# Kernel optimization log

Hardware: AMD Instinct MI355X
Metric: run time of the kernel (lower is better)

The kernel has to match this reference:

```python
import jax, jax.numpy as jnp
import numpy as np

ALPHA1 = 0.1   # rank margin
ALPHA2 = 5.0   # penalty scale when violated
ALPHA3 = 10.0  # sigmoid sharpness
ALPHA_OTHER = 0.5  # floor for top-k threshold


def setup_inputs() -> dict:
    key = jax.random.key(0)
    B, C, L, S = 4096, 9605, 8, 50  # batch, classes, whitelist labels, classes per label
    k1, k2, k3 = jax.random.split(key, 3)
    x = jax.random.normal(k1, (B, C), dtype=jnp.float32)
    # sparse multi-label binarized targets (~10 positives/sample)
    y = (jax.random.uniform(k2, (B, C)) < 0.001).astype(jnp.float32)
    y_neg = (jax.random.uniform(k3, (B, C)) < 0.001).astype(jnp.float32)
    # disjoint per-label whitelist class index sets -> [L, C] boolean masks
    rng = np.random.default_rng(0)
    idx = rng.choice(C, size=L * S, replace=False).reshape(L, S)
    wl = np.zeros((L, C), dtype=bool)
    wl[np.arange(L)[:, None], idx] = True
    return {"x": x, "y": y, "y_neg": y_neg, "wl_mask": jnp.asarray(wl)}


def reference(x, y, y_neg, wl_mask):
    # x, y, y_neg: [B, C]; wl_mask: [L, C] bool. Returns scalar loss_rank_all.sum().
    # (The per-element BCE `loss` tensor and find_gt_whitelist(y_neg) in the
    #  original are dead code w.r.t. the returned value and are omitted.)
    xs = jax.nn.sigmoid(x)                                   # [B, C]
    wl_f = wl_mask.astype(x.dtype)                           # [L, C]
    # gt label present iff sum of y over that label's whitelist indices > 0
    gt_mask = (y @ wl_f.T) > 0                               # [B, L]
    has_gt = jnp.any(gt_mask, axis=1)                        # [B]
    first_gt = jnp.argmax(gt_mask, axis=1)                   # [B] first gt label
    # x_sorted[15] (16th largest) via top_k instead of full sort
    top16 = jax.lax.top_k(xs, 16)[0][:, 15]                  # [B]
    thres = jnp.maximum(top16, ALPHA_OTHER)                  # [B]
    # ---- branch: no gt whitelist label ----
    union = jnp.any(wl_mask, axis=0)                         # [C]
    x2_no = jnp.max(jnp.where(union[None, :], xs, -jnp.inf), axis=1)
    x1_no = thres
    # ---- branch: has gt whitelist label ----
    samp_mask = wl_mask[first_gt]                            # [B, C]
    x1_gt = jnp.max(jnp.where(samp_mask, xs, -jnp.inf), axis=1)
    L = wl_mask.shape[0]
    # faithful to original: indexes xs at LABEL positions 0..L-1, init 0
    non_gt = jnp.max(jnp.where(~gt_mask, xs[:, :L], 0.0), axis=1, initial=0.0)
    x2_gt = jnp.maximum(non_gt, thres)
    # ---- select branch and apply our_rank_loss ----
    x1 = jnp.where(has_gt, x1_gt, x1_no)
    x2 = jnp.where(has_gt, x2_gt, x2_no)
    d = x2 - x1 + ALPHA1
    sig = jax.nn.sigmoid(ALPHA3 * d)
    rank = jnp.where(d > 0, ALPHA2 * sig, sig)
    return jnp.sum(rank)
```

## Files before the change

### kernel.cpp

```cpp
#include <hip/hip_runtime.h>
#include <stdint.h>

#define BLOCK 512
#define CAP 512
#define LISTCAP 2048
#define WS_ROUT 2560
static constexpr int LBL = 8;

#define A1 0.1f
#define A2 5.0f
#define A3 10.0f

__device__ __forceinline__ unsigned b2key(unsigned u) {
  return (u & 0x80000000u) ? ~u : (u | 0x80000000u);
}
__device__ __forceinline__ unsigned f2key(float f) { return b2key(__float_as_uint(f)); }
__device__ __forceinline__ float key2f(unsigned k) {
  unsigned u = (k & 0x80000000u) ? (k & 0x7FFFFFFFu) : ~k;
  return __uint_as_float(u);
}
__device__ __forceinline__ float sigm(float v) { return 1.0f / (1.0f + __expf(-v)); }

__global__ void detect_kernel(const unsigned char* __restrict__ wl, int total,
                              int* __restrict__ ws) {
  int i = blockIdx.x * 256 + threadIdx.x;
  if (i < total && (i & 3) != 0 && wl[i] == 1) atomicOr(&ws[1], 1);
}

__global__ void build_kernel(const unsigned char* __restrict__ wl, int C, int total,
                             int* __restrict__ ws) {
  int i = blockIdx.x * 256 + threadIdx.x;
  if (i >= total) return;
  bool v = ws[1] ? (wl[i] != 0) : (((const int*)wl)[i] != 0);
  if (v) {
    int p = atomicAdd(&ws[0], 1);
    if (p < LISTCAP) ws[2 + p] = ((i / C) << 16) | (i % C);
  }
}

__global__ __launch_bounds__(BLOCK, 8) void rank_kernel(
    const float* __restrict__ x, const float* __restrict__ y,
    const int* __restrict__ wsl, float* __restrict__ rout, int C) {
  __shared__ unsigned hist[2048];
  __shared__ unsigned buf[CAP];
  __shared__ float wtop2[BLOCK / 64];
  __shared__ unsigned wtot[BLOCK / 64];
  __shared__ unsigned lmaxk[LBL];
  __shared__ float smL[LBL];
  __shared__ unsigned gtbits, bufcnt, s_seld, s_selk, s_selc, s_key;

  int tid = threadIdx.x;
  int row = blockIdx.x;
  long long base = (long long)row * C;
  const float* __restrict__ xr = x + base;
  const float* __restrict__ yr = y + base;

  if (tid < LBL) lmaxk[tid] = 0u;
  if (tid == 0) { gtbits = 0u; bufcnt = 0u; }

  int s = (int)((4 - (base & 3)) & 3);
  int nv = (C - s) >> 2;
  int tail0 = s + 4 * nv;
  int nrem = C - 4 * nv;

  const float4* __restrict__ xv4 = (const float4*)(xr + s);
  float4 f[5];
  bool hv[5];
#pragma unroll
  for (int t = 0; t < 5; ++t) {
    int i = tid + t * BLOCK;
    hv[t] = (i < nv);
    f[t] = hv[t] ? xv4[i] : make_float4(-INFINITY, -INFINITY, -INFINITY, -INFINITY);
  }
  float tailv = -INFINITY;
  bool havet = false;
  if (tid < nrem) {
    int c = (tid < s) ? tid : tail0 + (tid - s);
    tailv = xr[c];
    havet = true;
  }
  if (tid < LBL) smL[tid] = xr[tid];

  int cnt = wsl[0];
  if (cnt > LISTCAP) cnt = LISTCAP;
  for (int j = tid; j < cnt; j += BLOCK) {
    int pk = wsl[2 + j];
    int c = pk & 0xFFFF, l = pk >> 16;
    float yv = yr[c];
    unsigned xk = f2key(xr[c]);
    if (yv != 0.0f) atomicOr(&gtbits, 1u << l);
    atomicMax(&lmaxk[l], xk);
  }

  float tmax = tailv;
#pragma unroll
  for (int t = 0; t < 5; ++t)
    tmax = fmaxf(tmax, fmaxf(fmaxf(f[t].x, f[t].y), fmaxf(f[t].z, f[t].w)));

  float a1 = tmax, a2 = -INFINITY;
#pragma unroll
  for (int st = 1; st < 64; st <<= 1) {
    float b1 = __shfl_xor(a1, st, 64);
    float b2 = __shfl_xor(a2, st, 64);
    float m = fminf(a1, b1);
    float o = (a1 >= b1) ? a2 : b2;
    a1 = fmaxf(a1, b1);
    a2 = fmaxf(m, o);
  }
  int w = tid >> 6;
  if ((tid & 63) == 0) wtop2[w] = a2;
  __syncthreads();
  float p = wtop2[0];
#pragma unroll
  for (int i = 1; i < BLOCK / 64; ++i) p = fminf(p, wtop2[i]);

#pragma unroll
  for (int t = 0; t < 5; ++t) {
    if (f[t].x >= p) { unsigned q = atomicAdd(&bufcnt, 1u); if (q < CAP) buf[q] = f2key(f[t].x); }
    if (f[t].y >= p) { unsigned q = atomicAdd(&bufcnt, 1u); if (q < CAP) buf[q] = f2key(f[t].y); }
    if (f[t].z >= p) { unsigned q = atomicAdd(&bufcnt, 1u); if (q < CAP) buf[q] = f2key(f[t].z); }
    if (f[t].w >= p) { unsigned q = atomicAdd(&bufcnt, 1u); if (q < CAP) buf[q] = f2key(f[t].w); }
  }
  if (havet && tailv >= p) { unsigned q = atomicAdd(&bufcnt, 1u); if (q < CAP) buf[q] = f2key(tailv); }
  __syncthreads();

  unsigned selkey = 0u;
  int bc = (int)bufcnt;
  if (bc >= 16 && bc <= CAP) {
    unsigned mk = (tid < bc) ? buf[tid] : 0u;
    int g = 0, e2 = 0;
    for (int j = 0; j < bc; ++j) {
      unsigned bk = buf[j];
      g += (bk > mk);
      e2 += (bk == mk);
    }
    if (tid < bc && g < 16 && 16 <= g + e2) s_key = mk;
    __syncthreads();
    selkey = s_key;
  } else {
    unsigned prefix = 0, pmask = 0;
    int k = 16;
    bool done = false;
    const int SHa[3] = {21, 10, 0};
    const int WIDa[3] = {11, 11, 10};
    for (int lev = 0; lev < 3 && !done; ++lev) {
      int shift = SHa[lev];
      int nb = 1 << WIDa[lev];
      unsigned bmask = (unsigned)nb - 1u;
      for (int i = tid; i < nb; i += BLOCK) hist[i] = 0;
      if (tid == 0) bufcnt = 0;
      __syncthreads();
#pragma unroll
      for (int t = 0; t < 5; ++t)
        if (hv[t]) {
          unsigned kk[4] = {f2key(f[t].x), f2key(f[t].y), f2key(f[t].z), f2key(f[t].w)};
#pragma unroll
          for (int e = 0; e < 4; ++e)
            if ((kk[e] & pmask) == prefix) atomicAdd(&hist[(kk[e] >> shift) & bmask], 1u);
        }
      if (havet) {
        unsigned tk = f2key(tailv);
        if ((tk & pmask) == prefix) atomicAdd(&hist[(tk >> shift) & bmask], 1u);
      }
      __syncthreads();
      int bpt = nb / BLOCK;
      int b0 = tid * bpt;
      unsigned cs = 0;
      for (int b = 0; b < bpt; ++b) cs += hist[b0 + b];
      unsigned v = cs;
      int lane = tid & 63;
#pragma unroll
      for (int st = 1; st < 64; st <<= 1) {
        unsigned tv = __shfl_down(v, st, 64);
        if (lane + st < 64) v += tv;
      }
      int w2 = tid >> 6;
      if (lane == 0) wtot[w2] = v;
      __syncthreads();
      unsigned above = 0;
      for (int ww = w2 + 1; ww < BLOCK / 64; ++ww) above += wtot[ww];
      unsigned S_incl = v + above;
      unsigned S_excl = S_incl - cs;
      if (S_excl < (unsigned)k && (unsigned)k <= S_incl) {
        int kk2 = k - (int)S_excl;
        int d = b0 + bpt - 1;
        for (; d > b0; --d) {
          int cb = (int)hist[d];
          if (kk2 <= cb) break;
          kk2 -= cb;
        }
        s_seld = (unsigned)d;
        s_selk = (unsigned)kk2;
        s_selc = hist[d];
      }
      __syncthreads();
      prefix |= s_seld << shift;
      pmask |= bmask << shift;
      k = (int)s_selk;
      unsigned selc = s_selc;
      if (lev == 2) {
        selkey = prefix;
        done = true;
      } else if (selc <= (unsigned)CAP) {
#pragma unroll
        for (int t = 0; t < 5; ++t)
          if (hv[t]) {
            unsigned kk[4] = {f2key(f[t].x), f2key(f[t].y), f2key(f[t].z), f2key(f[t].w)};
#pragma unroll
            for (int e = 0; e < 4; ++e)
              if ((kk[e] & pmask) == prefix) {
                unsigned q = atomicAdd(&bufcnt, 1u);
                if (q < CAP) buf[q] = kk[e];
              }
          }
        if (havet) {
          unsigned tk = f2key(tailv);
          if ((tk & pmask) == prefix) {
            unsigned q = atomicAdd(&bufcnt, 1u);
            if (q < CAP) buf[q] = tk;
          }
        }
        __syncthreads();
        int bc2 = (int)bufcnt;
        if (bc2 > CAP) bc2 = CAP;
        unsigned mk = (tid < bc2) ? buf[tid] : 0u;
        int g = 0, e2 = 0;
        for (int j = 0; j < bc2; ++j) {
          unsigned bk = buf[j];
          g += (bk > mk);
          e2 += (bk == mk);
        }
        if (tid < bc2 && g < k && k <= g + e2) s_key = mk;
        __syncthreads();
        selkey = s_key;
        done = true;
      }
    }
  }

  if (tid == 0) {
    float x16 = key2f(selkey);
    float thres = sigm(fmaxf(x16, 0.0f));
    unsigned gb = gtbits;
    float x1, x2;
    if (gb) {
      int first = __ffs((int)gb) - 1;
      x1 = sigm(key2f(lmaxk[first]));
      float ng = 0.0f;
      for (int l = 0; l < LBL; ++l)
        if (!((gb >> l) & 1)) ng = fmaxf(ng, sigm(smL[l]));
      x2 = fmaxf(ng, thres);
    } else {
      unsigned um = 0;
      for (int l = 0; l < LBL; ++l) um = um > lmaxk[l] ? um : lmaxk[l];
      x1 = thres;
      x2 = sigm(key2f(um));
    }
    float dd = x2 - x1 + A1;
    float sg = 1.0f / (1.0f + __expf(-A3 * dd));
    rout[row] = (dd > 0.0f) ? A2 * sg : sg;
  }
}

__global__ __launch_bounds__(256) void reduce_kernel(const float* __restrict__ rin,
                                                     float* __restrict__ out, int B) {
  __shared__ float smr[256];
  float acc = 0.0f;
  for (int i = threadIdx.x; i < B; i += 256) acc += rin[i];
  smr[threadIdx.x] = acc;
  __syncthreads();
  for (int st = 128; st > 0; st >>= 1) {
    if (threadIdx.x < st) smr[threadIdx.x] += smr[threadIdx.x + st];
    __syncthreads();
  }
  if (threadIdx.x == 0) out[0] = smr[0];
}

extern "C" void kernel_launch(void* const* d_in, const int* in_sizes, int n_in,
                              void* d_out, int out_size, void* d_ws, size_t ws_size,
                              hipStream_t stream) {
  const float* x = (const float*)d_in[0];
  const float* y = (const float*)d_in[1];
  const unsigned char* wl = (const unsigned char*)d_in[3];

  int C = in_sizes[3] / LBL;
  int B = in_sizes[0] / C;
  int total = LBL * C;
  int* ws = (int*)d_ws;

  hipMemsetAsync(d_ws, 0, 8, stream);
  int nbs = (total + 255) / 256;
  hipLaunchKernelGGL(detect_kernel, dim3(nbs), dim3(256), 0, stream, wl, total, ws);
  hipLaunchKernelGGL(build_kernel, dim3(nbs), dim3(256), 0, stream, wl, C, total, ws);

  hipLaunchKernelGGL(rank_kernel, dim3(B), dim3(BLOCK), 0, stream, x, y, ws,
                     (float*)(ws + WS_ROUT), C);
  hipLaunchKernelGGL(reduce_kernel, dim3(1), dim3(256), 0, stream,
                     (const float*)(ws + WS_ROUT), (float*)d_out, B);
}
```

Before: 69.39 us.

## Replace whitelist index list with per-class label byte map read alongside x

Swaps the sparse list of (label, class) pairs for a per-class byte table giving each class's whitelist label. Four copies are stored, one per alignment shift, so each row can read the table as 32-bit words matching its float4 loads of x. Each thread now updates the label maxima and gt bits from values it already holds in registers instead of doing scattered gather loads. The rank-16 selection over the candidate buffer is also limited to one wavefront looping over elements. The cost is an extra coalesced read of table words per row, plus y loads for any vector that touches a whitelisted class.

```diff
diff --git a/kernel.cpp b/kernel.cpp
--- a/kernel.cpp
+++ b/kernel.cpp
@@ -3,18 +3,19 @@
 
 #define BLOCK 512
 #define CAP 512
-#define LISTCAP 2048
-#define WS_ROUT 2560
+#define TBL0 16
+#define TBLW 2408
+#define WS_ROUT 10240
 static constexpr int LBL = 8;
 
 #define A1 0.1f
 #define A2 5.0f
 #define A3 10.0f
 
-__device__ __forceinline__ unsigned b2key(unsigned u) {
+__device__ __forceinline__ unsigned f2key(float f) {
+  unsigned u = __float_as_uint(f);
   return (u & 0x80000000u) ? ~u : (u | 0x80000000u);
 }
-__device__ __forceinline__ unsigned f2key(float f) { return b2key(__float_as_uint(f)); }
 __device__ __forceinline__ float key2f(unsigned k) {
   unsigned u = (k & 0x80000000u) ? (k & 0x7FFFFFFFu) : ~k;
   return __uint_as_float(u);
@@ -27,20 +28,33 @@
   if (i < total && (i & 3) != 0 && wl[i] == 1) atomicOr(&ws[1], 1);
 }
 
-__global__ void build_kernel(const unsigned char* __restrict__ wl, int C, int total,
-                             int* __restrict__ ws) {
-  int i = blockIdx.x * 256 + threadIdx.x;
-  if (i >= total) return;
-  bool v = ws[1] ? (wl[i] != 0) : (((const int*)wl)[i] != 0);
-  if (v) {
-    int p = atomicAdd(&ws[0], 1);
-    if (p < LISTCAP) ws[2 + p] = ((i / C) << 16) | (i % C);
+__global__ void build_lmap(const unsigned char* __restrict__ wl, int C,
+                           int* __restrict__ ws) {
+  int c = blockIdx.x * 256 + threadIdx.x;
+  if (c >= C) return;
+  int isByte = ws[1];
+  unsigned lab = 255u;
+  if (isByte) {
+    for (int l = 0; l < LBL; ++l)
+      if (wl[(long long)l * C + c]) lab = (unsigned)l;
+  } else {
+    const int* w = (const int*)wl;
+    for (int l = 0; l < LBL; ++l)
+      if (w[(long long)l * C + c]) lab = (unsigned)l;
+  }
+  if (lab < (unsigned)LBL) {
+#pragma unroll
+    for (int s2 = 0; s2 < 4; ++s2)
+      if (c >= s2) {
+        unsigned char* tb = (unsigned char*)(ws + TBL0 + s2 * TBLW);
+        tb[c - s2] = (unsigned char)lab;
+      }
   }
 }
 
 __global__ __launch_bounds__(BLOCK, 8) void rank_kernel(
     const float* __restrict__ x, const float* __restrict__ y,
-    const int* __restrict__ wsl, float* __restrict__ rout, int C) {
+    const int* __restrict__ ws, float* __restrict__ rout, int C) {
   __shared__ unsigned hist[2048];
   __shared__ unsigned buf[CAP];
   __shared__ float wtop2[BLOCK / 64];
@@ -55,41 +69,63 @@
   const float* __restrict__ xr = x + base;
   const float* __restrict__ yr = y + base;
 
-  if (tid < LBL) lmaxk[tid] = 0u;
-  if (tid == 0) { gtbits = 0u; bufcnt = 0u; }
-
   int s = (int)((4 - (base & 3)) & 3);
   int nv = (C - s) >> 2;
   int tail0 = s + 4 * nv;
   int nrem = C - 4 * nv;
 
+  const unsigned* Ts = (const unsigned*)(ws + TBL0 + s * TBLW);
+  const unsigned char* Tb = (const unsigned char*)Ts;
+  const unsigned char* T0b = (const unsigned char*)(ws + TBL0);
+
   const float4* __restrict__ xv4 = (const float4*)(xr + s);
+  const float4* __restrict__ yv4 = (const float4*)(yr + s);
   float4 f[5];
   bool hv[5];
+  unsigned lw[5];
 #pragma unroll
   for (int t = 0; t < 5; ++t) {
     int i = tid + t * BLOCK;
     hv[t] = (i < nv);
     f[t] = hv[t] ? xv4[i] : make_float4(-INFINITY, -INFINITY, -INFINITY, -INFINITY);
+    lw[t] = hv[t] ? Ts[i] : 0xFFFFFFFFu;
   }
   float tailv = -INFINITY;
   bool havet = false;
+  unsigned tlab = 255u;
+  int tc = 0;
   if (tid < nrem) {
-    int c = (tid < s) ? tid : tail0 + (tid - s);
-    tailv = xr[c];
+    tc = (tid < s) ? tid : tail0 + (tid - s);
+    tailv = xr[tc];
     havet = true;
+    tlab = (tid < s) ? (unsigned)T0b[tc] : (unsigned)Tb[tc - s];
   }
   if (tid < LBL) smL[tid] = xr[tid];
 
-  int cnt = wsl[0];
-  if (cnt > LISTCAP) cnt = LISTCAP;
-  for (int j = tid; j < cnt; j += BLOCK) {
-    int pk = wsl[2 + j];
-    int c = pk & 0xFFFF, l = pk >> 16;
-    float yv = yr[c];
-    unsigned xk = f2key(xr[c]);
-    if (yv != 0.0f) atomicOr(&gtbits, 1u << l);
-    atomicMax(&lmaxk[l], xk);
+  if (tid < LBL) lmaxk[tid] = 0u;
+  if (tid == 0) { gtbits = 0u; bufcnt = 0u; }
+  __syncthreads();
+
+#pragma unroll
+  for (int t = 0; t < 5; ++t) {
+    if (lw[t] != 0xFFFFFFFFu) {
+      float4 yv = yv4[tid + t * BLOCK];
+      unsigned w2 = lw[t];
+      float fe[4] = {f[t].x, f[t].y, f[t].z, f[t].w};
+      float ye[4] = {yv.x, yv.y, yv.z, yv.w};
+#pragma unroll
+      for (int e = 0; e < 4; ++e) {
+        unsigned lab = (w2 >> (8 * e)) & 255u;
+        if (lab < (unsigned)LBL) {
+          atomicMax(&lmaxk[lab], f2key(fe[e]));
+          if (ye[e] != 0.0f) atomicOr(&gtbits, 1u << lab);
+        }
+      }
+    }
+  }
+  if (havet && tlab < (unsigned)LBL) {
+    atomicMax(&lmaxk[tlab], f2key(tailv));
+    if (yr[tc] != 0.0f) atomicOr(&gtbits, 1u << tlab);
   }
 
   float tmax = tailv;
@@ -127,14 +163,18 @@
   unsigned selkey = 0u;
   int bc = (int)bufcnt;
   if (bc >= 16 && bc <= CAP) {
-    unsigned mk = (tid < bc) ? buf[tid] : 0u;
-    int g = 0, e2 = 0;
-    for (int j = 0; j < bc; ++j) {
-      unsigned bk = buf[j];
-      g += (bk > mk);
-      e2 += (bk == mk);
+    if (tid < 64) {
+      for (int i = tid; i < bc; i += 64) {
+        unsigned mk = buf[i];
+        int g = 0, e2 = 0;
+        for (int j = 0; j < bc; ++j) {
+          unsigned bk = buf[j];
+          g += (bk > mk);
+          e2 += (bk == mk);
+        }
+        if (g < 16 && 16 <= g + e2) s_key = mk;
+      }
     }
-    if (tid < bc && g < 16 && 16 <= g + e2) s_key = mk;
     __syncthreads();
     selkey = s_key;
   } else {
@@ -288,10 +328,12 @@
   int total = LBL * C;
   int* ws = (int*)d_ws;
 
-  hipMemsetAsync(d_ws, 0, 8, stream);
+  hipMemsetAsync(d_ws, 0, TBL0 * 4, stream);
+  hipMemsetAsync(ws + TBL0, 0xFF, (size_t)4 * TBLW * 4, stream);
   int nbs = (total + 255) / 256;
   hipLaunchKernelGGL(detect_kernel, dim3(nbs), dim3(256), 0, stream, wl, total, ws);
-  hipLaunchKernelGGL(build_kernel, dim3(nbs), dim3(256), 0, stream, wl, C, total, ws);
+  int nbc = (C + 255) / 256;
+  hipLaunchKernelGGL(build_lmap, dim3(nbc), dim3(256), 0, stream, wl, C, ws);
 
   hipLaunchKernelGGL(rank_kernel, dim3(B), dim3(BLOCK), 0, stream, x, y, ws,
                      (float*)(ws + WS_ROUT), C);
```

Result: slower. 76.71 us (+10.6%).

## Prefetch whitelist gathers alongside row loads; restrict top-16 rank scan to one wave

Applied to the files above, without the earlier changes.

The whitelist list is pre-filled with -1 sentinels so each thread unconditionally loads two list entries. Their x/y gathers are issued together with the row's float4 loads instead of in a separate loop after them, which lets the gather latency overlap. The O(n^2) rank selection over the candidate buffer now runs on a single 64-thread wave that loops over the candidates, so the other waves skip the redundant LDS scans. This costs an extra memset of the sentinel list and a fixed list capacity of 1024 entries.

```diff
diff --git a/kernel.cpp b/kernel.cpp
--- a/kernel.cpp
+++ b/kernel.cpp
@@ -2,19 +2,21 @@
 #include <stdint.h>
 
 #define BLOCK 512
+#define NW 5
 #define CAP 512
-#define LISTCAP 2048
-#define WS_ROUT 2560
+#define LISTCAP 1024
+#define WS_LIST 8
+#define WS_ROUT 4096
 static constexpr int LBL = 8;
 
 #define A1 0.1f
 #define A2 5.0f
 #define A3 10.0f
 
-__device__ __forceinline__ unsigned b2key(unsigned u) {
+__device__ __forceinline__ unsigned f2key(float f) {
+  unsigned u = __float_as_uint(f);
   return (u & 0x80000000u) ? ~u : (u | 0x80000000u);
 }
-__device__ __forceinline__ unsigned f2key(float f) { return b2key(__float_as_uint(f)); }
 __device__ __forceinline__ float key2f(unsigned k) {
   unsigned u = (k & 0x80000000u) ? (k & 0x7FFFFFFFu) : ~k;
   return __uint_as_float(u);
@@ -34,13 +36,13 @@
   bool v = ws[1] ? (wl[i] != 0) : (((const int*)wl)[i] != 0);
   if (v) {
     int p = atomicAdd(&ws[0], 1);
-    if (p < LISTCAP) ws[2 + p] = ((i / C) << 16) | (i % C);
+    if (p < LISTCAP) ws[WS_LIST + p] = ((i / C) << 16) | (i % C);
   }
 }
 
 __global__ __launch_bounds__(BLOCK, 8) void rank_kernel(
     const float* __restrict__ x, const float* __restrict__ y,
-    const int* __restrict__ wsl, float* __restrict__ rout, int C) {
+    const int* __restrict__ ws, float* __restrict__ rout, int C) {
   __shared__ unsigned hist[2048];
   __shared__ unsigned buf[CAP];
   __shared__ float wtop2[BLOCK / 64];
@@ -55,19 +57,16 @@
   const float* __restrict__ xr = x + base;
   const float* __restrict__ yr = y + base;
 
-  if (tid < LBL) lmaxk[tid] = 0u;
-  if (tid == 0) { gtbits = 0u; bufcnt = 0u; }
-
   int s = (int)((4 - (base & 3)) & 3);
   int nv = (C - s) >> 2;
   int tail0 = s + 4 * nv;
   int nrem = C - 4 * nv;
 
   const float4* __restrict__ xv4 = (const float4*)(xr + s);
-  float4 f[5];
-  bool hv[5];
-#pragma unroll
-  for (int t = 0; t < 5; ++t) {
+  float4 f[NW];
+  bool hv[NW];
+#pragma unroll
+  for (int t = 0; t < NW; ++t) {
     int i = tid + t * BLOCK;
     hv[t] = (i < nv);
     f[t] = hv[t] ? xv4[i] : make_float4(-INFINITY, -INFINITY, -INFINITY, -INFINITY);
@@ -80,21 +79,30 @@
     havet = true;
   }
   if (tid < LBL) smL[tid] = xr[tid];
-
-  int cnt = wsl[0];
-  if (cnt > LISTCAP) cnt = LISTCAP;
-  for (int j = tid; j < cnt; j += BLOCK) {
-    int pk = wsl[2 + j];
-    int c = pk & 0xFFFF, l = pk >> 16;
-    float yv = yr[c];
-    unsigned xk = f2key(xr[c]);
-    if (yv != 0.0f) atomicOr(&gtbits, 1u << l);
-    atomicMax(&lmaxk[l], xk);
+  int e0 = ws[WS_LIST + tid];
+  int e1 = ws[WS_LIST + BLOCK + tid];
+  float xg0 = 0.0f, yg0 = 0.0f, xg1 = 0.0f, yg1 = 0.0f;
+  if (e0 != -1) { int c = e0 & 0xFFFF; xg0 = xr[c]; yg0 = yr[c]; }
+  if (e1 != -1) { int c = e1 & 0xFFFF; xg1 = xr[c]; yg1 = yr[c]; }
+
+  if (tid < LBL) lmaxk[tid] = 0u;
+  if (tid == 0) { gtbits = 0u; bufcnt = 0u; }
+  __syncthreads();
+
+  if (e0 != -1) {
+    int l = e0 >> 16;
+    atomicMax(&lmaxk[l], f2key(xg0));
+    if (yg0 != 0.0f) atomicOr(&gtbits, 1u << l);
+  }
+  if (e1 != -1) {
+    int l = e1 >> 16;
+    atomicMax(&lmaxk[l], f2key(xg1));
+    if (yg1 != 0.0f) atomicOr(&gtbits, 1u << l);
   }
 
   float tmax = tailv;
 #pragma unroll
-  for (int t = 0; t < 5; ++t)
+  for (int t = 0; t < NW; ++t)
     tmax = fmaxf(tmax, fmaxf(fmaxf(f[t].x, f[t].y), fmaxf(f[t].z, f[t].w)));
 
   float a1 = tmax, a2 = -INFINITY;
@@ -115,7 +123,7 @@
   for (int i = 1; i < BLOCK / 64; ++i) p = fminf(p, wtop2[i]);
 
 #pragma unroll
-  for (int t = 0; t < 5; ++t) {
+  for (int t = 0; t < NW; ++t) {
     if (f[t].x >= p) { unsigned q = atomicAdd(&bufcnt, 1u); if (q < CAP) buf[q] = f2key(f[t].x); }
     if (f[t].y >= p) { unsigned q = atomicAdd(&bufcnt, 1u); if (q < CAP) buf[q] = f2key(f[t].y); }
     if (f[t].z >= p) { unsigned q = atomicAdd(&bufcnt, 1u); if (q < CAP) buf[q] = f2key(f[t].z); }
@@ -127,14 +135,18 @@
   unsigned selkey = 0u;
   int bc = (int)bufcnt;
   if (bc >= 16 && bc <= CAP) {
-    unsigned mk = (tid < bc) ? buf[tid] : 0u;
-    int g = 0, e2 = 0;
-    for (int j = 0; j < bc; ++j) {
-      unsigned bk = buf[j];
-      g += (bk > mk);
-      e2 += (bk == mk);
+    if (tid < 64) {
+      for (int i = tid; i < bc; i += 64) {
+        unsigned mk = buf[i];
+        int g = 0, e2 = 0;
+        for (int j = 0; j < bc; ++j) {
+          unsigned bk = buf[j];
+          g += (bk > mk);
+          e2 += (bk == mk);
+        }
+        if (g < 16 && 16 <= g + e2) s_key = mk;
+      }
     }
-    if (tid < bc && g < 16 && 16 <= g + e2) s_key = mk;
     __syncthreads();
     selkey = s_key;
   } else {
@@ -151,7 +163,7 @@
       if (tid == 0) bufcnt = 0;
       __syncthreads();
 #pragma unroll
-      for (int t = 0; t < 5; ++t)
+      for (int t = 0; t < NW; ++t)
         if (hv[t]) {
           unsigned kk[4] = {f2key(f[t].x), f2key(f[t].y), f2key(f[t].z), f2key(f[t].w)};
 #pragma unroll
@@ -203,7 +215,7 @@
         done = true;
       } else if (selc <= (unsigned)CAP) {
 #pragma unroll
-        for (int t = 0; t < 5; ++t)
+        for (int t = 0; t < NW; ++t)
           if (hv[t]) {
             unsigned kk[4] = {f2key(f[t].x), f2key(f[t].y), f2key(f[t].z), f2key(f[t].w)};
 #pragma unroll
@@ -288,7 +300,8 @@
   int total = LBL * C;
   int* ws = (int*)d_ws;
 
-  hipMemsetAsync(d_ws, 0, 8, stream);
+  hipMemsetAsync(ws, 0, WS_LIST * 4, stream);
+  hipMemsetAsync(ws + WS_LIST, 0xFF, (size_t)LISTCAP * 4, stream);
   int nbs = (total + 255) / 256;
   hipLaunchKernelGGL(detect_kernel, dim3(nbs), dim3(256), 0, stream, wl, total, ws);
   hipLaunchKernelGGL(build_kernel, dim3(nbs), dim3(256), 0, stream, wl, C, total, ws);
```

Result: slower. 72.11 us (+3.9%).
